# Kernel optimization log

Hardware: AMD Instinct MI355X
Metric: run time of the kernel (lower is better)

Reference implementation:

```python
import jax, jax.numpy as jnp
import numpy as np

B, S, D = 8, 2048, 256
C, H = 32, 4
HD = D // H  # head_dim = 64


def setup_inputs() -> dict:
    key = jax.random.key(0)
    ks = jax.random.split(key, 12)
    scale = 0.02
    x = jax.random.normal(ks[0], (B, S, D), dtype=jnp.float32)
    conditioning = jax.random.uniform(ks[1], (B, S, C), dtype=jnp.float32)
    Wq_w = jax.random.normal(ks[2], (D, D), dtype=jnp.float32) * scale
    Wq_b = jax.random.normal(ks[3], (D,), dtype=jnp.float32) * scale
    Wv_w = jax.random.normal(ks[4], (D, D), dtype=jnp.float32) * scale
    Wv_b = jax.random.normal(ks[5], (D,), dtype=jnp.float32) * scale
    Wk_w = jax.random.normal(ks[6], (C, D, D), dtype=jnp.float32) * scale  # stacked per-class torch Linear weights [out,in]
    Wk_b = jax.random.normal(ks[7], (C, D), dtype=jnp.float32) * scale
    Wo_w = jax.random.normal(ks[8], (D, D), dtype=jnp.float32) * scale
    Wo_b = jax.random.normal(ks[9], (D,), dtype=jnp.float32) * scale
    return {"x": x, "conditioning": conditioning,
            "Wq_w": Wq_w, "Wq_b": Wq_b, "Wv_w": Wv_w, "Wv_b": Wv_b,
            "Wk_w": Wk_w, "Wk_b": Wk_b, "Wo_w": Wo_w, "Wo_b": Wo_b}


def reference(x, conditioning, Wq_w, Wq_b, Wv_w, Wv_b, Wk_w, Wk_b, Wo_w, Wo_b):
    # torch Linear: y = x @ W.T + b, with W of shape [out, in]
    q = (x @ Wq_w.T + Wq_b).reshape(B, S, H, HD).transpose(0, 2, 1, 3)  # (B,H,S,HD)
    v = (x @ Wv_w.T + Wv_b).reshape(B, S, H, HD).transpose(0, 2, 1, 3)
    # per-class keys: (B,C,S,D)
    class_keys = jnp.einsum('bsd,cfd->bcsf', x, Wk_w) + Wk_b[None, :, None, :]
    # data-dependent weighted sum over classes -> effective key (B,S,D)
    k = jnp.einsum('bsc,bcsf->bsf', conditioning, class_keys)
    k = k.reshape(B, S, H, HD).transpose(0, 2, 1, 3)  # (B,H,S,HD)
    # scaled dot-product attention (dropout_p = 0)
    scale = 1.0 / jnp.sqrt(jnp.float32(HD))
    scores = jnp.einsum('bhqd,bhkd->bhqk', q, k) * scale
    attn = jax.nn.softmax(scores, axis=-1)
    out = jnp.einsum('bhqk,bhkd->bhqd', attn, v)
    out = out.transpose(0, 2, 1, 3).reshape(B, S, D)
    return out @ Wo_w.T + Wo_b
```

## Files before the change

kernel.cpp:

```cpp
#include <hip/hip_runtime.h>
#include <hip/hip_bf16.h>

#define BB 8
#define SS 2048
#define DD 256
#define CC 32
#define HH 4
#define HD 64
#define MTOT (BB*SS)

using bf16    = __hip_bfloat16;
using short8  = __attribute__((ext_vector_type(8))) short;
using short4v = __attribute__((ext_vector_type(4))) short;
using floatx4 = __attribute__((ext_vector_type(4))) float;

#if __has_builtin(__builtin_amdgcn_mfma_f32_16x16x16_bf16)
  #define MFMA_PV16(a,b,c) __builtin_amdgcn_mfma_f32_16x16x16_bf16(a,b,c,0,0,0)
  #define HAVE_PV16 1
#elif __has_builtin(__builtin_amdgcn_mfma_f32_16x16x16bf16_1k)
  #define MFMA_PV16(a,b,c) __builtin_amdgcn_mfma_f32_16x16x16bf16_1k(a,b,c,0,0,0)
  #define HAVE_PV16 1
#else
  #define HAVE_PV16 0
#endif

#if __has_builtin(__builtin_amdgcn_global_load_lds)
  #define HAVE_GLL 1
#else
  #define HAVE_GLL 0
#endif

__device__ inline float bf2f(unsigned short u) {
    union { unsigned int i; float f; } v; v.i = ((unsigned int)u) << 16; return v.f;
}
__device__ inline unsigned short f2bfbits(float f) {
    bf16 h = __float2bfloat16(f);
    return __builtin_bit_cast(unsigned short, h);
}

#define N_X    (MTOT*DD)
#define N_COND (MTOT*CC)
#define N_WQW  (DD*DD)
#define N_WQB  (DD)
#define N_WVW  (DD*DD)
#define N_WVB  (DD)
#define N_WKW  (CC*DD*DD)
#define N_WKB  (CC*DD)
#define N_WOW  (DD*DD)
#define N_WOB  (DD)
#define P0 0
#define P1 (P0+N_X)
#define P2 (P1+N_COND)
#define P3 (P2+N_WQW)
#define P4 (P3+N_WQB)
#define P5 (P4+N_WVW)
#define P6 (P5+N_WVB)
#define P7 (P6+N_WKW)
#define P8 (P7+N_WKB)
#define P9 (P8+N_WOW)
#define PTOT (P9+N_WOB)

__global__ void convert_all(const void* s0, const void* s1, const void* s2,
                            const void* s3, const void* s4, const void* s5,
                            const void* s6, const void* s7, const void* s8,
                            const void* s9, bf16* dst, int* flagw)
{
    __shared__ int cnts[4];
    {
        const float* xf = (const float*)s0;
        float v = fabsf(xf[threadIdx.x]);
        bool ok = (v == v) && v > 1e-4f && v < 1e4f;
        unsigned long long m = __ballot(ok);
        if ((threadIdx.x & 63) == 0) cnts[threadIdx.x >> 6] = __popcll(m);
    }
    __syncthreads();
    const bool f32 = (cnts[0] + cnts[1] + cnts[2] + cnts[3]) > 128;
    if (blockIdx.x == 0 && threadIdx.x == 0) *flagw = f32 ? 1 : 0;

    size_t i = ((size_t)blockIdx.x * 256 + threadIdx.x) * 8;
    const size_t stride = (size_t)gridDim.x * 256 * 8;
    for (; i < (size_t)PTOT; i += stride) {
        const void* src; size_t off;
        if      (i < P1) { src = s0; off = i - P0; }
        else if (i < P2) { src = s1; off = i - P1; }
        else if (i < P3) { src = s2; off = i - P2; }
        else if (i < P4) { src = s3; off = i - P3; }
        else if (i < P5) { src = s4; off = i - P4; }
        else if (i < P6) { src = s5; off = i - P5; }
        else if (i < P7) { src = s6; off = i - P6; }
        else if (i < P8) { src = s7; off = i - P7; }
        else if (i < P9) { src = s8; off = i - P8; }
        else             { src = s9; off = i - P9; }
        if (f32) {
            const float* s = (const float*)src + off;
            float4 a = *(const float4*)(s);
            float4 b = *(const float4*)(s + 4);
            __align__(16) unsigned short t[8];
            t[0] = f2bfbits(a.x); t[1] = f2bfbits(a.y);
            t[2] = f2bfbits(a.z); t[3] = f2bfbits(a.w);
            t[4] = f2bfbits(b.x); t[5] = f2bfbits(b.y);
            t[6] = f2bfbits(b.z); t[7] = f2bfbits(b.w);
            *(uint4*)(dst + i) = *(const uint4*)t;
        } else {
            *(uint4*)(dst + i) = *(const uint4*)((const unsigned short*)src + off);
        }
    }
}

__device__ __forceinline__ void gemm_body(const bf16* __restrict__ X, const bf16* __restrict__ W,
                                          const bf16* __restrict__ bias, void* __restrict__ Yv,
                                          const int* __restrict__ flagp, int flex_out, int vt_out,
                                          unsigned short* smem, int m0, int n0)
{
    const int LDT = 264;
    unsigned short* xs = smem;
    unsigned short* ws = smem + 64 * 264;
    const int t = threadIdx.x;

    for (int i = 0; i < 8; ++i) {
        int c = t + i * 256;
        int row = c >> 5, col = (c & 31) * 8;
        *(uint4*)&xs[row * LDT + col] = *(const uint4*)(X + (size_t)(m0 + row) * DD + col);
        *(uint4*)&ws[row * LDT + col] = *(const uint4*)(W + (size_t)(n0 + row) * DD + col);
    }
    __syncthreads();

    const int w = t >> 6, lane = t & 63;
    const int lrow = lane & 15, lk = (lane >> 4) * 8, rgrp = (lane >> 4) * 4;
    floatx4 acc[4] = {};
    const unsigned short* ax = &xs[(w * 16 + lrow) * LDT + lk];
    for (int kt = 0; kt < 8; ++kt) {
        short8 a = *(const short8*)(ax + kt * 32);
        #pragma unroll
        for (int j = 0; j < 4; ++j) {
            short8 b = *(const short8*)&ws[(j * 16 + lrow) * LDT + kt * 32 + lk];
            acc[j] = __builtin_amdgcn_mfma_f32_16x16x32_bf16(a, b, acc[j], 0, 0, 0);
        }
    }

    if (vt_out) {
        __syncthreads();
        unsigned short* ts = xs;
        #pragma unroll
        for (int j = 0; j < 4; ++j) {
            float bv = __bfloat162float(bias[n0 + j * 16 + lrow]);
            #pragma unroll
            for (int r = 0; r < 4; ++r)
                ts[(j * 16 + lrow) * 72 + w * 16 + rgrp + r] = f2bfbits(acc[j][r] + bv);
        }
        __syncthreads();
        const int bq = m0 >> 11, s0v = m0 & 2047, h = n0 >> 6;
        bf16* dstb = (bf16*)Yv + ((size_t)(bq * HH + h) * HD) * SS + s0v;
        for (int i = 0; i < 2; ++i) {
            int idx = t + i * 256, row = idx >> 3, ch = (idx & 7) * 8;
            *(uint4*)(dstb + (size_t)row * SS + ch) = *(const uint4*)&ts[row * 72 + ch];
        }
        return;
    }

    const bool f32o = flex_out && (*flagp != 0);
    #pragma unroll
    for (int j = 0; j < 4; ++j) {
        int col = n0 + j * 16 + lrow;
        float bv = __bfloat162float(bias[col]);
        #pragma unroll
        for (int r = 0; r < 4; ++r) {
            int row = m0 + w * 16 + rgrp + r;
            float val = acc[j][r] + bv;
            if (f32o) ((float*)Yv)[(size_t)row * DD + col] = val;
            else      ((bf16*)Yv)[(size_t)row * DD + col] = __float2bfloat16(val);
        }
    }
}

__launch_bounds__(256, 2)
__global__ void gemm_qv(const bf16* __restrict__ X,
                        const bf16* __restrict__ Wqw, const bf16* __restrict__ Wqb, bf16* __restrict__ Qout,
                        const bf16* __restrict__ Wvw, const bf16* __restrict__ Wvb, bf16* __restrict__ Vout,
                        const int* __restrict__ flagp)
{
    __shared__ __align__(16) unsigned short smem[2 * 64 * 264];
    int gi = blockIdx.x;
    if (gi < 1024) {
        int n0 = (gi & 3) * 64, m0 = (gi >> 2) * 64;
        gemm_body(X, Wqw, Wqb, (void*)Qout, flagp, 0, 0, smem, m0, n0);
    } else {
        gi -= 1024;
        int n0 = (gi & 3) * 64, m0 = (gi >> 2) * 64;
        gemm_body(X, Wvw, Wvb, (void*)Vout, flagp, 0, 1, smem, m0, n0);
    }
}

__launch_bounds__(256, 2)
__global__ void gemm_bias(const bf16* __restrict__ X, const bf16* __restrict__ W,
                          const bf16* __restrict__ bias, void* __restrict__ Yv,
                          const int* __restrict__ flagp, int flex_out, int vt_out)
{
    __shared__ __align__(16) unsigned short smem[2 * 64 * 264];
    gemm_body(X, W, bias, Yv, flagp, flex_out, vt_out, smem, blockIdx.y * 64, blockIdx.x * 64);
}

__device__ __forceinline__ void stage_ws4(const bf16* __restrict__ Wc,
                                          unsigned short* wsbuf, int w, int lane)
{
    #pragma unroll
    for (int i = 0; i < 8; ++i) {
        int rr = w * 16 + i * 2 + (lane >> 5);
        int cs = (lane & 31) ^ (rr & 7);
        const bf16* src = Wc + (size_t)rr * DD + cs * 8;
        unsigned short* dst = wsbuf + (size_t)(w * 16 + i * 2) * DD;
#if HAVE_GLL
        __builtin_amdgcn_global_load_lds(
            (const __attribute__((address_space(1))) void*)src,
            (__attribute__((address_space(3))) void*)dst, 16, 0, 0);
#else
        uint4 v = *(const uint4*)src;
        *(uint4*)(dst + (size_t)lane * 8) = v;
#endif
    }
}

#define WS_HALF (64 * 256)
#define CONDS_OFF 65536
#define KBST_OFF  75776
#define SMEM_BYTES 80896

__launch_bounds__(256, 2)
__global__ void classkey(const bf16* __restrict__ X, const bf16* __restrict__ Cond,
                         const bf16* __restrict__ Wk, const bf16* __restrict__ Wkb,
                         bf16* __restrict__ Kout)
{
    __shared__ __align__(16) unsigned char smem[SMEM_BYTES];
    unsigned short* wsbase = (unsigned short*)smem;
    unsigned short* conds  = (unsigned short*)(smem + CONDS_OFF);
    unsigned short* kbsT   = (unsigned short*)(smem + KBST_OFF);

    const int t    = threadIdx.x;
    const int w    = t >> 6;
    const int lane = t & 63;
    const int r16  = lane & 15;
    const int quad = lane >> 4;
    const int mw   = w & 1;
    const int kw   = w >> 1;
    const int m0   = blockIdx.y * 128;
    const int n0   = blockIdx.x * 64;

    {
        int row = t >> 1, c16 = (t & 1) * 16;
        *(uint4*)&conds[row * 40 + c16]     = *(const uint4*)(Cond + (size_t)(m0 + row) * CC + c16);
        *(uint4*)&conds[row * 40 + c16 + 8] = *(const uint4*)(Cond + (size_t)(m0 + row) * CC + c16 + 8);
    }
    {
        int f = t >> 2, cbase = (t & 3) * 8;
        #pragma unroll
        for (int e = 0; e < 8; ++e)
            kbsT[f * 40 + cbase + e] =
                __builtin_bit_cast(unsigned short, Wkb[(size_t)(cbase + e) * DD + n0 + f]);
    }

    short8 xa[4][4];
    #pragma unroll
    for (int mt = 0; mt < 4; ++mt) {
        const bf16* xrow = X + (size_t)(m0 + mw * 64 + mt * 16 + r16) * DD + kw * 128 + quad * 8;
        #pragma unroll
        for (int kt = 0; kt < 4; ++kt)
            xa[mt][kt] = *(const short8*)(xrow + kt * 32);
    }

    stage_ws4(Wk + (size_t)n0 * DD, wsbase, w, lane);

    floatx4 acck[4][4] = {};
    for (int c = 0; c < CC; ++c) {
        __syncthreads();
        if (c + 1 < CC)
            stage_ws4(Wk + (size_t)(c + 1) * DD * DD + (size_t)n0 * DD,
                      wsbase + ((c + 1) & 1) * WS_HALF, w, lane);

        const unsigned short* wb = wsbase + (c & 1) * WS_HALF;
        floatx4 p[4][4];
        #pragma unroll
        for (int kt = 0; kt < 4; ++kt) {
            short8 bj[4];
            #pragma unroll
            for (int j = 0; j < 4; ++j)
                bj[j] = *(const short8*)&wb[(j * 16 + r16) * DD +
                          (((kw * 16 + kt * 4 + quad) ^ (r16 & 7)) << 3)];
            if (kt == 0) {
                floatx4 z = {};
                #pragma unroll
                for (int mt = 0; mt < 4; ++mt)
                    #pragma unroll
                    for (int j = 0; j < 4; ++j)
                        p[mt][j] = __builtin_amdgcn_mfma_f32_16x16x32_bf16(xa[mt][0], bj[j], z, 0, 0, 0);
            } else {
                #pragma unroll
                for (int mt = 0; mt < 4; ++mt)
                    #pragma unroll
                    for (int j = 0; j < 4; ++j)
                        p[mt][j] = __builtin_amdgcn_mfma_f32_16x16x32_bf16(xa[mt][kt], bj[j], p[mt][j], 0, 0, 0);
            }
        }
        #pragma unroll
        for (int mt = 0; mt < 4; ++mt)
            #pragma unroll
            for (int r = 0; r < 4; ++r) {
                float cv = bf2f(conds[(mw * 64 + mt * 16 + quad * 4 + r) * 40 + c]);
                #pragma unroll
                for (int j = 0; j < 4; ++j) acck[mt][j][r] += cv * p[mt][j][r];
            }
    }

    if (kw == 0) {
        #pragma unroll
        for (int mt = 0; mt < 4; ++mt) {
            short8 ac = *(const short8*)&conds[(mw * 64 + mt * 16 + r16) * 40 + quad * 8];
            #pragma unroll
            for (int j = 0; j < 4; ++j) {
                short8 bc = *(const short8*)&kbsT[(j * 16 + r16) * 40 + quad * 8];
                acck[mt][j] = __builtin_amdgcn_mfma_f32_16x16x32_bf16(ac, bc, acck[mt][j], 0, 0, 0);
            }
        }
    }

    float* red = (float*)smem;
    __syncthreads();
    #pragma unroll
    for (int mt = 0; mt < 4; ++mt)
        #pragma unroll
        for (int j = 0; j < 4; ++j)
            #pragma unroll
            for (int r = 0; r < 4; ++r)
                red[(kw * 128 + mw * 64 + mt * 16 + quad * 4 + r) * 65 + j * 16 + r16] =
                    acck[mt][j][r];
    __syncthreads();
    {
        int row = t >> 1, cg = (t & 1) * 32;
        __align__(16) unsigned short outv[32];
        #pragma unroll
        for (int cc = 0; cc < 32; ++cc) {
            float s = red[(size_t)row * 65 + cg + cc] + red[(size_t)(128 + row) * 65 + cg + cc];
            outv[cc] = f2bfbits(s);
        }
        bf16* dst = Kout + (size_t)(m0 + row) * DD + n0 + cg;
        #pragma unroll
        for (int u = 0; u < 4; ++u)
            *(uint4*)(dst + u * 8) = *(const uint4*)&outv[u * 8];
    }
}

__device__ inline void stage_kv(const bf16* __restrict__ kRow,
                                const bf16* __restrict__ vRow,
                                unsigned short* kbuf, unsigned short* vbuf,
                                int w, int lane)
{
    int r  = w * 8 + (lane >> 3);
    int cs = (lane & 7) ^ (r & 7);
#if HAVE_GLL
    __builtin_amdgcn_global_load_lds(
        (const __attribute__((address_space(1))) void*)(kRow + (size_t)r * DD + cs * 8),
        (__attribute__((address_space(3))) void*)(kbuf + w * 512), 16, 0, 0);
    __builtin_amdgcn_global_load_lds(
        (const __attribute__((address_space(1))) void*)(vRow + (size_t)r * SS + cs * 8),
        (__attribute__((address_space(3))) void*)(vbuf + w * 512), 16, 0, 0);
#else
    *(uint4*)(kbuf + w * 512 + (size_t)lane * 8) = *(const uint4*)(kRow + (size_t)r * DD + cs * 8);
    *(uint4*)(vbuf + w * 512 + (size_t)lane * 8) = *(const uint4*)(vRow + (size_t)r * SS + cs * 8);
#endif
}

__launch_bounds__(512, 4)
__global__ void attn(const bf16* __restrict__ Q, const bf16* __restrict__ Kb,
                     const bf16* __restrict__ VT, bf16* __restrict__ O)
{
    __shared__ __align__(16) unsigned short ks[2][64 * 64];
    __shared__ __align__(16) unsigned short vt[2][64 * 64];
#if !HAVE_PV16
    __shared__ __align__(16) unsigned short ps[128 * 72];
#endif
    const int t    = threadIdx.x;
    const int w    = t >> 6;
    const int lane = t & 63;
    const int r16  = lane & 15;
    const int quad = lane >> 4;
    const int bh   = blockIdx.y;
    const int b    = bh >> 2, h = bh & 3;
    const int q0   = blockIdx.x * 128;
    const size_t base  = ((size_t)b * SS) * DD + h * HD;
    const size_t vbase = (size_t)bh * HD * SS;

    short8 qa[2];
    {
        const bf16* qrow = Q + base + (size_t)(q0 + w * 16 + r16) * DD + quad * 8;
        #pragma unroll
        for (int k2 = 0; k2 < 2; ++k2) {
            short8 raw = *(const short8*)(qrow + k2 * 32);
            short8 sc;
            #pragma unroll
            for (int e = 0; e < 8; ++e)
                sc[e] = (short)f2bfbits(bf2f((unsigned short)raw[e]) * 0.125f);
            qa[k2] = sc;
        }
    }

    stage_kv(Kb + base, VT + vbase, &ks[0][0], &vt[0][0], w, lane);

    floatx4 acco[4] = {};
    float mrun = -1e30f, lrun = 0.f;

    for (int kt = 0; kt < SS / 64; ++kt) {
        __syncthreads();
        if (kt + 1 < SS / 64)
            stage_kv(Kb + base + (size_t)(kt + 1) * 64 * DD,
                     VT + vbase + (size_t)(kt + 1) * 64,
                     &ks[(kt + 1) & 1][0], &vt[(kt + 1) & 1][0], w, lane);

        const unsigned short* kbuf = &ks[kt & 1][0];
        const unsigned short* vbuf = &vt[kt & 1][0];

        floatx4 s[4] = {};
        #pragma unroll
        for (int k2 = 0; k2 < 2; ++k2) {
            short8 bq = qa[k2];
            #pragma unroll
            for (int j = 0; j < 4; ++j) {
                short8 ak = *(const short8*)&kbuf[(j * 16 + r16) * 64 +
                                                  (((k2 * 4 + quad) ^ (r16 & 7)) << 3)];
                s[j] = __builtin_amdgcn_mfma_f32_16x16x32_bf16(ak, bq, s[j], 0, 0, 0);
            }
        }

        float mx = -1e30f;
        #pragma unroll
        for (int j = 0; j < 4; ++j)
            #pragma unroll
            for (int r = 0; r < 4; ++r) mx = fmaxf(mx, s[j][r]);
        mx = fmaxf(mx, __shfl_xor(mx, 16, 64));
        mx = fmaxf(mx, __shfl_xor(mx, 32, 64));
        float mnew  = fmaxf(mrun, mx);
        float alpha = __expf(mrun - mnew);
        float sum = 0.f;
        #pragma unroll
        for (int j = 0; j < 4; ++j)
            #pragma unroll
            for (int r = 0; r < 4; ++r) {
                float e = __expf(s[j][r] - mnew);
                s[j][r] = e; sum += e;
            }
        sum += __shfl_xor(sum, 16, 64);
        sum += __shfl_xor(sum, 32, 64);
        lrun = lrun * alpha + sum;
        mrun = mnew;

        #pragma unroll
        for (int r = 0; r < 4; ++r) {
            float ar = __shfl(alpha, (quad << 4) + quad * 4 + r, 64);
            #pragma unroll
            for (int jn = 0; jn < 4; ++jn) acco[jn][r] *= ar;
        }

#if HAVE_PV16
        #pragma unroll
        for (int j = 0; j < 4; ++j) {
            short4v p;
            p[0] = (short)f2bfbits(s[j][0]); p[1] = (short)f2bfbits(s[j][1]);
            p[2] = (short)f2bfbits(s[j][2]); p[3] = (short)f2bfbits(s[j][3]);
            #pragma unroll
            for (int jn = 0; jn < 4; ++jn) {
                short4v vv = *(const short4v*)&vbuf[(jn * 16 + r16) * 64 +
                                                    ((((j * 2) + (quad >> 1)) ^ (r16 & 7)) << 3) +
                                                    (quad & 1) * 4];
                acco[jn] = MFMA_PV16(p, vv, acco[jn]);
            }
        }
#else
        #pragma unroll
        for (int j = 0; j < 4; ++j)
            #pragma unroll
            for (int r = 0; r < 4; ++r)
                ps[(w * 16 + r16) * 72 + j * 16 + quad * 4 + r] = f2bfbits(s[j][r]);
        #pragma unroll
        for (int k2 = 0; k2 < 2; ++k2) {
            short8 a = *(const short8*)&ps[(w * 16 + r16) * 72 + k2 * 32 + quad * 8];
            #pragma unroll
            for (int jn = 0; jn < 4; ++jn) {
                short8 bb = *(const short8*)&vbuf[(jn * 16 + r16) * 64 +
                                                  (((k2 * 4 + quad) ^ (r16 & 7)) << 3)];
                acco[jn] = __builtin_amdgcn_mfma_f32_16x16x32_bf16(a, bb, acco[jn], 0, 0, 0);
            }
        }
#endif
    }

    #pragma unroll
    for (int r = 0; r < 4; ++r) {
        float lr = __shfl(lrun, (quad << 4) + quad * 4 + r, 64);
        float inv = 1.0f / lr;
        int row = q0 + w * 16 + quad * 4 + r;
        #pragma unroll
        for (int jn = 0; jn < 4; ++jn)
            O[base + (size_t)row * DD + jn * 16 + r16] = __float2bfloat16(acco[jn][r] * inv);
    }
}

extern "C" void kernel_launch(void* const* d_in, const int* in_sizes, int n_in,
                              void* d_out, int out_size, void* d_ws, size_t ws_size,
                              hipStream_t stream)
{
    int*  flag = (int*)d_ws;
    bf16* conv = (bf16*)((char*)d_ws + 256);

    const bf16* xb    = conv + P0;
    const bf16* condb = conv + P1;
    const bf16* wqw   = conv + P2;
    const bf16* wqb   = conv + P3;
    const bf16* wvw   = conv + P4;
    const bf16* wvb   = conv + P5;
    const bf16* wkw   = conv + P6;
    const bf16* wkb   = conv + P7;
    const bf16* wow   = conv + P8;
    const bf16* wob   = conv + P9;

    bf16* qb = conv + PTOT;
    bf16* kb = qb + (size_t)MTOT * DD;
    bf16* vb = kb + (size_t)MTOT * DD;
    bf16* ob = vb + (size_t)MTOT * DD;

    dim3 blk(256);
    hipLaunchKernelGGL(convert_all, dim3((PTOT / 8 + 255) / 256), blk, 0, stream,
                       d_in[0], d_in[1], d_in[2], d_in[3], d_in[4],
                       d_in[5], d_in[6], d_in[7], d_in[8], d_in[9],
                       conv, flag);

    dim3 gck(DD / 64, MTOT / 128);
    hipLaunchKernelGGL(classkey, gck, blk, 0, stream, xb, condb, wkw, wkb, kb);

    hipLaunchKernelGGL(gemm_qv, dim3(2048), blk, 0, stream,
                       xb, wqw, wqb, qb, wvw, wvb, vb, flag);

    dim3 ga(SS / 128, BB * HH);
    hipLaunchKernelGGL(attn, ga, dim3(512), 0, stream, qb, kb, vb, ob);

    dim3 gg(DD / 64, MTOT / 64);
    hipLaunchKernelGGL(gemm_bias, gg, blk, 0, stream, ob, wow, wob, d_out, flag, 1, 0);
}
```

Baseline: 244.2 us.

## Use exp2 softmax with lazy rescaling and MFMA row-sum accumulation

Folds log2(e) into the Q prescale so the softmax uses native exp2. The running max is only updated and the accumulators rescaled when some row's max grows by more than 8, which skips most rescale shuffles. The row sum is computed by an extra MFMA against a ones vector instead of a VALU sum with cross-lane shuffles, and a max3 tree shortens the max reduction. The costs are one extra MFMA per tile and the risk of larger exponent values under lazy rescaling. The row sum is also taken from the bf16-rounded probabilities.

Measured after the change: 232.7 us. 1.05x faster.

```diff
diff --git a/kernel.cpp b/kernel.cpp
--- a/kernel.cpp
+++ b/kernel.cpp
@@ -30,12 +30,21 @@
   #define HAVE_GLL 0
 #endif
 
+#if __has_builtin(__builtin_amdgcn_exp2f)
+  #define EXP2F(x) __builtin_amdgcn_exp2f(x)
+#else
+  #define EXP2F(x) exp2f(x)
+#endif
+
 __device__ inline float bf2f(unsigned short u) {
     union { unsigned int i; float f; } v; v.i = ((unsigned int)u) << 16; return v.f;
 }
 __device__ inline unsigned short f2bfbits(float f) {
     bf16 h = __float2bfloat16(f);
     return __builtin_bit_cast(unsigned short, h);
+}
+__device__ inline float max3f(float a, float b, float c) {
+    return fmaxf(fmaxf(a, b), c);
 }
 
 #define N_X    (MTOT*DD)
@@ -388,6 +397,7 @@
     const size_t base  = ((size_t)b * SS) * DD + h * HD;
     const size_t vbase = (size_t)bh * HD * SS;
 
+    const float QSC = 0.125f * 1.4426950408889634f;
     short8 qa[2];
     {
         const bf16* qrow = Q + base + (size_t)(q0 + w * 16 + r16) * DD + quad * 8;
@@ -397,7 +407,7 @@
             short8 sc;
             #pragma unroll
             for (int e = 0; e < 8; ++e)
-                sc[e] = (short)f2bfbits(bf2f((unsigned short)raw[e]) * 0.125f);
+                sc[e] = (short)f2bfbits(bf2f((unsigned short)raw[e]) * QSC);
             qa[k2] = sc;
         }
     }
@@ -405,7 +415,16 @@
     stage_kv(Kb + base, VT + vbase, &ks[0][0], &vt[0][0], w, lane);
 
     floatx4 acco[4] = {};
-    float mrun = -1e30f, lrun = 0.f;
+    floatx4 accl = {};
+    float mrun = -1e30f;
+
+#if HAVE_PV16
+    const short4v ones4 = { (short)0x3F80, (short)0x3F80, (short)0x3F80, (short)0x3F80 };
+#else
+    short8 ones8;
+    #pragma unroll
+    for (int e = 0; e < 8; ++e) ones8[e] = (short)0x3F80;
+#endif
 
     for (int kt = 0; kt < SS / 64; ++kt) {
         __syncthreads();
@@ -429,34 +448,33 @@
             }
         }
 
-        float mx = -1e30f;
-        #pragma unroll
-        for (int j = 0; j < 4; ++j)
-            #pragma unroll
-            for (int r = 0; r < 4; ++r) mx = fmaxf(mx, s[j][r]);
+        float g0 = max3f(s[0][0], s[0][1], s[0][2]);
+        float g1 = max3f(s[0][3], s[1][0], s[1][1]);
+        float g2 = max3f(s[1][2], s[1][3], s[2][0]);
+        float g3 = max3f(s[2][1], s[2][2], s[2][3]);
+        float g4 = max3f(s[3][0], s[3][1], s[3][2]);
+        float mx = fmaxf(max3f(g0, g1, g2), max3f(g3, g4, s[3][3]));
         mx = fmaxf(mx, __shfl_xor(mx, 16, 64));
         mx = fmaxf(mx, __shfl_xor(mx, 32, 64));
-        float mnew  = fmaxf(mrun, mx);
-        float alpha = __expf(mrun - mnew);
-        float sum = 0.f;
+
+        if (__any(mx > mrun + 8.0f)) {
+            float mnew  = fmaxf(mrun, mx);
+            float alpha = EXP2F(mrun - mnew);
+            mrun = mnew;
+            #pragma unroll
+            for (int r = 0; r < 4; ++r) {
+                float ar = __shfl(alpha, (quad << 4) + quad * 4 + r, 64);
+                #pragma unroll
+                for (int jn = 0; jn < 4; ++jn) acco[jn][r] *= ar;
+                accl[r] *= ar;
+            }
+        }
+
         #pragma unroll
         for (int j = 0; j < 4; ++j)
             #pragma unroll
-            for (int r = 0; r < 4; ++r) {
-                float e = __expf(s[j][r] - mnew);
-                s[j][r] = e; sum += e;
-            }
-        sum += __shfl_xor(sum, 16, 64);
-        sum += __shfl_xor(sum, 32, 64);
-        lrun = lrun * alpha + sum;
-        mrun = mnew;
-
-        #pragma unroll
-        for (int r = 0; r < 4; ++r) {
-            float ar = __shfl(alpha, (quad << 4) + quad * 4 + r, 64);
-            #pragma unroll
-            for (int jn = 0; jn < 4; ++jn) acco[jn][r] *= ar;
-        }
+            for (int r = 0; r < 4; ++r)
+                s[j][r] = EXP2F(s[j][r] - mrun);
 
 #if HAVE_PV16
         #pragma unroll
@@ -464,6 +482,7 @@
             short4v p;
             p[0] = (short)f2bfbits(s[j][0]); p[1] = (short)f2bfbits(s[j][1]);
             p[2] = (short)f2bfbits(s[j][2]); p[3] = (short)f2bfbits(s[j][3]);
+            accl = MFMA_PV16(p, ones4, accl);
             #pragma unroll
             for (int jn = 0; jn < 4; ++jn) {
                 short4v vv = *(const short4v*)&vbuf[(jn * 16 + r16) * 64 +
@@ -481,6 +500,7 @@
         #pragma unroll
         for (int k2 = 0; k2 < 2; ++k2) {
             short8 a = *(const short8*)&ps[(w * 16 + r16) * 72 + k2 * 32 + quad * 8];
+            accl = __builtin_amdgcn_mfma_f32_16x16x32_bf16(a, ones8, accl, 0, 0, 0);
             #pragma unroll
             for (int jn = 0; jn < 4; ++jn) {
                 short8 bb = *(const short8*)&vbuf[(jn * 16 + r16) * 64 +
@@ -493,8 +513,7 @@
 
     #pragma unroll
     for (int r = 0; r < 4; ++r) {
-        float lr = __shfl(lrun, (quad << 4) + quad * 4 + r, 64);
-        float inv = 1.0f / lr;
+        float inv = 1.0f / accl[r];
         int row = q0 + w * 16 + quad * 4 + r;
         #pragma unroll
         for (int jn = 0; jn < 4; ++jn)
```
